# Optimization experiments

Measured on AMD Instinct MI355X. Metric: run time of the kernel, lower is better.

## Reference

```python
import jax, jax.numpy as jnp
import numpy as np

B, Q, K, D, H = 4, 2048, 2048, 512, 8
DH = D // H
MASK_VAL = -1e6


def setup_inputs() -> dict:
    key = jax.random.key(0)
    ks = jax.random.split(key, 8)
    queries = jax.random.normal(ks[0], (B, Q, D), dtype=jnp.float32)
    keys = jax.random.normal(ks[1], (B, K, D), dtype=jnp.float32)
    values = jax.random.normal(ks[2], (B, K, D), dtype=jnp.float32)
    valid_lens = jax.random.randint(ks[3], (B,), 1, K + 1, dtype=jnp.int32)
    # torch nn.Linear weights: shape [out_features, in_features], y = x @ W.T
    s = 1.0 / np.sqrt(D)
    W_q = jax.random.uniform(ks[4], (D, D), jnp.float32, -s, s)
    W_k = jax.random.uniform(ks[5], (D, D), jnp.float32, -s, s)
    W_v = jax.random.uniform(ks[6], (D, D), jnp.float32, -s, s)
    W_o = jax.random.uniform(ks[7], (D, D), jnp.float32, -s, s)
    return {"queries": queries, "keys": keys, "values": values,
            "valid_lens": valid_lens, "W_q": W_q, "W_k": W_k,
            "W_v": W_v, "W_o": W_o}


def _split_heads(x):
    # [B, S, D] -> [B, H, S, DH]
    b, s, _ = x.shape
    return x.reshape(b, s, H, DH).transpose(0, 2, 1, 3)


def reference(queries, keys, values, valid_lens, W_q, W_k, W_v, W_o):
    q = _split_heads(queries @ W_q.T)   # [B,H,Q,DH]
    k = _split_heads(keys @ W_k.T)      # [B,H,K,DH]
    v = _split_heads(values @ W_v.T)    # [B,H,K,DH]
    scores = jnp.einsum("bhqd,bhkd->bhqk", q, k) / jnp.sqrt(jnp.float32(DH))
    # padding mask: key position < valid_len[b], broadcast over heads & queries
    mask = jnp.arange(K)[None, None, None, :] < valid_lens[:, None, None, None]
    scores = jnp.where(mask, scores, MASK_VAL)
    attn = jax.nn.softmax(scores, axis=-1)  # dropout=eval/no-op
    out = jnp.einsum("bhqk,bhkd->bhqd", attn, v)
    out = out.transpose(0, 2, 1, 3).reshape(queries.shape[0], q.shape[2], D)
    return out @ W_o.T
```

## Files before the change

### kernel.cpp

```cpp
#include <hip/hip_runtime.h>
#include <cstdint>
#include <cstddef>

#define BB  4
#define QQ  2048
#define SK  2048
#define DD  512
#define HH  8
#define DHH 64

typedef __bf16 bf16;
typedef bf16  bf16x8 __attribute__((ext_vector_type(8)));
typedef bf16  bf16x4 __attribute__((ext_vector_type(4)));
typedef float f32x4  __attribute__((ext_vector_type(4)));
typedef uint32_t u32x4 __attribute__((ext_vector_type(4)));

__device__ __forceinline__ void async16(void* lds, const void* g) {
  __builtin_amdgcn_global_load_lds(
      (const __attribute__((address_space(1))) unsigned int*)g,
      (__attribute__((address_space(3))) unsigned int*)lds, 16, 0, 0);
}

__device__ __forceinline__ uint32_t pk2(float lo, float hi) {
  return __builtin_amdgcn_perm(__builtin_bit_cast(uint32_t, hi),
                               __builtin_bit_cast(uint32_t, lo), 0x07060302u);
}

__global__ __launch_bounds__(256) void cvt_w(
    const float* __restrict__ w0, const float* __restrict__ w1,
    const float* __restrict__ w2, const float* __restrict__ w3,
    bf16* __restrict__ d0, bf16* __restrict__ d1, bf16* __restrict__ d2,
    bf16* __restrict__ d3, int nw4) {
  int i = blockIdx.x * 256 + threadIdx.x;
  const float* s;
  bf16* d;
  if (i < nw4)             { s = w0; d = d0; }
  else if (i < 2 * nw4)    { s = w1; d = d1; i -= nw4; }
  else if (i < 3 * nw4)    { s = w2; d = d2; i -= 2 * nw4; }
  else if (i < 4 * nw4)    { s = w3; d = d3; i -= 3 * nw4; }
  else return;
  float4 vv = ((const float4*)s)[i];
  bf16x4 o;
  o[0] = (bf16)vv.x; o[1] = (bf16)vv.y; o[2] = (bf16)vv.z; o[3] = (bf16)vv.w;
  ((bf16x4*)d)[i] = o;
}

template <int MT, int F32S, typename EpiF>
__device__ __forceinline__ void gemm_body(
    const bf16* __restrict__ A, const bf16* __restrict__ B,
    const float* __restrict__ Af, const float* __restrict__ Bf,
    int tM, int tN, EpiF epi_fn) {
  static_assert(F32S == 0 || MT == 4, "f32 staging assumes 4 chunks/thread");
  __shared__ __align__(16) bf16 lA[MT * 32 * 64];
  __shared__ __align__(16) bf16 lB[128 * 64];
  const int tid  = threadIdx.x;
  const int l    = tid & 63;
  const int w    = tid >> 6;
  const int lrow = l & 15, lq = l >> 4;
  const int wm = (w >> 1) * (MT * 16), wn = (w & 1) * 64;

  float4 rg[8];
  auto loadreg = [&](int it) {
    const int kt = it * 64;
#pragma unroll
    for (int j = 0; j < 4; ++j) {
      int c = j * 256 + tid, row = c >> 3, gcc = (c & 7) ^ (row & 7);
      const float* s = (F32S == 1)
          ? &Af[(size_t)(tM + row) * DD + kt + gcc * 8]
          : &Bf[(size_t)(tN + row) * DD + kt + gcc * 8];
      rg[2 * j]     = *(const float4*)s;
      rg[2 * j + 1] = *(const float4*)(s + 4);
    }
  };
  auto writereg = [&]() {
#pragma unroll
    for (int j = 0; j < 4; ++j) {
      int c = j * 256 + tid;
      float4 a = rg[2 * j], b2 = rg[2 * j + 1];
      bf16x8 o;
      o[0] = (bf16)a.x;  o[1] = (bf16)a.y;  o[2] = (bf16)a.z;  o[3] = (bf16)a.w;
      o[4] = (bf16)b2.x; o[5] = (bf16)b2.y; o[6] = (bf16)b2.z; o[7] = (bf16)b2.w;
      if constexpr (F32S == 1) *(bf16x8*)&lA[c * 8] = o;
      else                     *(bf16x8*)&lB[c * 8] = o;
    }
  };

  f32x4 acc[MT][4] = {};
  if constexpr (F32S) loadreg(0);
  for (int it = 0; it < 8; ++it) {
    const int kt = it * 64;
    if (it) __syncthreads();
    if constexpr (F32S != 1) {
#pragma unroll
      for (int j = 0; j < MT; ++j) {
        int c = j * 256 + tid, row = c >> 3, gcc = (c & 7) ^ (row & 7);
        async16(&lA[c * 8], &A[(size_t)(tM + row) * DD + kt + gcc * 8]);
      }
    }
    if constexpr (F32S != 2) {
#pragma unroll
      for (int j = 0; j < 4; ++j) {
        int c = j * 256 + tid, row = c >> 3, gcc = (c & 7) ^ (row & 7);
        async16(&lB[c * 8], &B[(size_t)(tN + row) * DD + kt + gcc * 8]);
      }
    }
    if constexpr (F32S) writereg();
    __syncthreads();
    if constexpr (F32S) {
      if (it + 1 < 8) loadreg(it + 1);
    }

#pragma unroll
    for (int ks = 0; ks < 2; ++ks) {
      bf16x8 af[MT], bfr[4];
#pragma unroll
      for (int mt = 0; mt < MT; ++mt) {
        int row = wm + mt * 16 + lrow;
        int chunk = row * 8 + ((ks * 4 + lq) ^ (lrow & 7));
        af[mt] = *(const bf16x8*)&lA[chunk * 8];
      }
#pragma unroll
      for (int nt = 0; nt < 4; ++nt) {
        int row = wn + nt * 16 + lrow;
        int chunk = row * 8 + ((ks * 4 + lq) ^ (lrow & 7));
        bfr[nt] = *(const bf16x8*)&lB[chunk * 8];
      }
#pragma unroll
      for (int mt = 0; mt < MT; ++mt)
#pragma unroll
        for (int nt = 0; nt < 4; ++nt)
          acc[mt][nt] = __builtin_amdgcn_mfma_f32_16x16x32_bf16(
              af[mt], bfr[nt], acc[mt][nt], 0, 0, 0);
    }
  }

#pragma unroll
  for (int mt = 0; mt < MT; ++mt)
#pragma unroll
    for (int nt = 0; nt < 4; ++nt) {
      int row0 = tM + wm + mt * 16 + lq * 4;
      int col  = tN + wn + nt * 16 + lrow;
      epi_fn(acc[mt][nt], row0, col);
    }
}

__global__ __launch_bounds__(256, 3) void proj3(
    const float* __restrict__ xq, const bf16* __restrict__ wq, bf16* __restrict__ qh,
    const float* __restrict__ xk, const bf16* __restrict__ wk, bf16* __restrict__ kh,
    const float* __restrict__ xv, const bf16* __restrict__ wv, bf16* __restrict__ vt,
    float qscale) {
  const int z = blockIdx.y, x = blockIdx.x;
  if (z < 2) {
    const bf16*  A = z == 0 ? wq : wk;
    const float* Bf = z == 0 ? xq : xk;
    bf16* Cout     = z == 0 ? qh : kh;
    const float scale = z == 0 ? qscale : 1.0f;
    int tM = (x & 3) * 128, tN = (x >> 2) * 128;
    gemm_body<4, 2>(A, nullptr, nullptr, Bf, tM, tN,
                    [&](const f32x4& a, int row0, int col) {
      int b2 = col >> 11, s = col & 2047;
      int h2 = row0 >> 6, dh0 = row0 & 63;
      bf16x4 o;
#pragma unroll
      for (int r = 0; r < 4; ++r) o[r] = (bf16)(a[r] * scale);
      *(bf16x4*)&Cout[((size_t)(b2 * HH + h2) * QQ + s) * DHH + dh0] = o;
    });
  } else {
    int tM = (x >> 2) * 128, tN = (x & 3) * 128;
    gemm_body<4, 1>(nullptr, wv, xv, nullptr, tM, tN,
                    [&](const f32x4& a, int row0, int col) {
      int b2 = row0 >> 11, s0 = row0 & 2047;
      int h2 = col >> 6,  dh = col & 63;
      int tile = s0 >> 6, kk = s0 & 63;
      int g = kk >> 4, a2 = (kk >> 2) & 3;
      int idx0 = ((g >> 1) * 4 + a2) * 8 + (g & 1) * 4;
      bf16x4 o;
#pragma unroll
      for (int r = 0; r < 4; ++r) o[r] = (bf16)a[r];
      *(bf16x4*)&vt[((size_t)(b2 * HH + h2) * DHH + dh) * SK + tile * 64 + idx0] = o;
    });
  }
}

__global__ __launch_bounds__(256, 3) void proj_o(
    const bf16* __restrict__ wo, const bf16* __restrict__ ao,
    float* __restrict__ Cout) {
  const int x = blockIdx.x;
  int tM = (x & 7) * 64, tN = (x >> 3) * 128;
  gemm_body<2, 0>(wo, ao, nullptr, nullptr, tM, tN,
                  [&](const f32x4& a, int row0, int col) {
    *(float4*)&Cout[(size_t)col * DD + row0] = *(const float4*)&a;
  });
}

__global__ __launch_bounds__(256, 3) void attn_fused(
    const bf16* __restrict__ qh, const bf16* __restrict__ kh,
    const bf16* __restrict__ vt, const int* __restrict__ valid_lens,
    bf16* __restrict__ ao) {
  __shared__ __align__(16) bf16 lK[3][64 * 64];
  __shared__ __align__(16) bf16 lV[3][64 * 64];
  const int tid  = threadIdx.x;
  const int l    = tid & 63;
  const int w    = tid >> 6;
  const int lrow = l & 15, lq = l >> 4;
  const int rx   = lrow & 7;
  const int bh = blockIdx.x;
  const int b = bh >> 3, h = bh & 7;
  const int qt = blockIdx.y;
  const int vl  = valid_lens[b];
  const int nkt = (vl + 63) >> 6;

  const int q0 = qt * 128 + w * 32;
  const bf16* qbase = qh + (size_t)bh * QQ * DHH;
  const bf16* kbase = kh + (size_t)bh * SK * DHH;
  const bf16* vbase = vt + (size_t)bh * DHH * SK;

  auto stageKV = [&](int k0, int buf) {
#pragma unroll
    for (int j = 0; j < 2; ++j) {
      int c = j * 256 + tid, row = c >> 3, gcc = (c & 7) ^ (row & 7);
      async16(&lK[buf][c * 8], &kbase[(size_t)(k0 + row) * DHH + gcc * 8]);
    }
#pragma unroll
    for (int j = 0; j < 2; ++j) {
      int c = j * 256 + tid, row = c >> 3, gcc = (c & 7) ^ (row & 7);
      async16(&lV[buf][c * 8], &vbase[(size_t)row * SK + k0 + gcc * 8]);
    }
  };

  bf16x8 qf[2][2];
#pragma unroll
  for (int g = 0; g < 2; ++g)
#pragma unroll
    for (int ks = 0; ks < 2; ++ks)
      qf[g][ks] = *(const bf16x8*)
          &qbase[(size_t)(q0 + g * 16 + lrow) * DHH + ks * 32 + lq * 8];

  f32x4 acc[2][4] = {};
  float rs[2] = {0.f, 0.f};

  stageKV(0, 0);
  asm volatile("s_waitcnt vmcnt(0)" ::: "memory");

  for (int kt = 0; kt < nkt; ++kt) {
    const int bi = kt % 3;
    if (kt + 1 < nkt) {
      stageKV((kt + 1) * 64, (kt + 1) % 3);
      asm volatile("s_waitcnt vmcnt(4)" ::: "memory");
    } else {
      asm volatile("s_waitcnt vmcnt(0)" ::: "memory");
    }
    __builtin_amdgcn_s_barrier();
    asm volatile("" ::: "memory");
    const bf16* bufK = lK[bi];
    const bf16* bufV = lV[bi];
    const int k0 = kt * 64;

    f32x4 s[2][4] = {};
    __builtin_amdgcn_s_setprio(1);
#pragma unroll
    for (int ks = 0; ks < 2; ++ks) {
#pragma unroll
      for (int t = 0; t < 4; ++t) {
        int row = t * 16 + lrow;
        int chunkc = row * 8 + ((ks * 4 + lq) ^ rx);
        bf16x8 kf = *(const bf16x8*)&bufK[chunkc * 8];
#pragma unroll
        for (int g = 0; g < 2; ++g)
          s[g][t] = __builtin_amdgcn_mfma_f32_16x16x32_bf16(
              kf, qf[g][ks], s[g][t], 0, 0, 0);
      }
    }
    __builtin_amdgcn_s_setprio(0);

    if (vl < k0 + 64) {
#pragma unroll
      for (int t = 0; t < 4; ++t) {
        int kb = k0 + t * 16 + lq * 4;
#pragma unroll
        for (int r = 0; r < 4; ++r)
          if (kb + r >= vl) { s[0][t][r] = -1e30f; s[1][t][r] = -1e30f; }
      }
    }

#pragma unroll
    for (int g = 0; g < 2; ++g)
#pragma unroll
      for (int t = 0; t < 4; ++t)
#pragma unroll
        for (int r = 0; r < 4; ++r) {
          float p = __builtin_amdgcn_exp2f(s[g][t][r]);
          rs[g] += p;
          s[g][t][r] = p;
        }

#pragma unroll
    for (int p2 = 0; p2 < 2; ++p2) {
      u32x4 pu[2];
#pragma unroll
      for (int g = 0; g < 2; ++g) {
        pu[g][0] = pk2(s[g][2 * p2][0], s[g][2 * p2][1]);
        pu[g][1] = pk2(s[g][2 * p2][2], s[g][2 * p2][3]);
        pu[g][2] = pk2(s[g][2 * p2 + 1][0], s[g][2 * p2 + 1][1]);
        pu[g][3] = pk2(s[g][2 * p2 + 1][2], s[g][2 * p2 + 1][3]);
      }
      bf16x8 pb0 = __builtin_bit_cast(bf16x8, pu[0]);
      bf16x8 pb1 = __builtin_bit_cast(bf16x8, pu[1]);
      int cc = (p2 * 4 + lq) ^ rx;
      __builtin_amdgcn_s_setprio(1);
#pragma unroll
      for (int mt = 0; mt < 4; ++mt) {
        int row = mt * 16 + lrow;
        bf16x8 vf = *(const bf16x8*)&bufV[(row * 8 + cc) * 8];
        acc[0][mt] = __builtin_amdgcn_mfma_f32_16x16x32_bf16(
            vf, pb0, acc[0][mt], 0, 0, 0);
        acc[1][mt] = __builtin_amdgcn_mfma_f32_16x16x32_bf16(
            vf, pb1, acc[1][mt], 0, 0, 0);
      }
      __builtin_amdgcn_s_setprio(0);
    }
  }

#pragma unroll
  for (int g = 0; g < 2; ++g) {
    rs[g] += __shfl_xor(rs[g], 16);
    rs[g] += __shfl_xor(rs[g], 32);
  }

#pragma unroll
  for (int g = 0; g < 2; ++g) {
    float inv = 1.0f / rs[g];
    int q = q0 + g * 16 + lrow;
#pragma unroll
    for (int mt = 0; mt < 4; ++mt) {
      bf16x4 o;
#pragma unroll
      for (int r = 0; r < 4; ++r) o[r] = (bf16)(acc[g][mt][r] * inv);
      *(bf16x4*)&ao[((size_t)(b * QQ + q)) * DD + h * DHH + mt * 16 + lq * 4] = o;
    }
  }
}

extern "C" void kernel_launch(void* const* d_in, const int* in_sizes, int n_in,
                              void* d_out, int out_size, void* d_ws, size_t ws_size,
                              hipStream_t stream) {
  const float* queries    = (const float*)d_in[0];
  const float* keys       = (const float*)d_in[1];
  const float* values     = (const float*)d_in[2];
  const int*   valid_lens = (const int*)d_in[3];
  const float* W_q = (const float*)d_in[4];
  const float* W_k = (const float*)d_in[5];
  const float* W_v = (const float*)d_in[6];
  const float* W_o = (const float*)d_in[7];

  const size_t NX = (size_t)BB * QQ * DD;
  const size_t NW = (size_t)DD * DD;

  bf16* wq = (bf16*)d_ws;
  bf16* wk = wq + NW;
  bf16* wv = wk + NW;
  bf16* wo = wv + NW;
  bf16* qh = wo + NW;
  bf16* kh = qh + NX;
  bf16* vt = kh + NX;
  bf16* ao = vt + NX;

  dim3 blk(256);
  const int nw4 = (int)(NW / 4);
  cvt_w<<<dim3((4 * nw4 + 255) / 256), blk, 0, stream>>>(
      W_q, W_k, W_v, W_o, wq, wk, wv, wo, nw4);

  const float qscale = 0.125f * 1.44269504088896340736f;
  proj3<<<dim3(256, 3), blk, 0, stream>>>(queries, wq, qh, keys, wk, kh,
                                          values, wv, vt, qscale);

  attn_fused<<<dim3(BB * HH, QQ / 128), blk, 0, stream>>>(
      qh, kh, vt, valid_lens, ao);

  proj_o<<<dim3(512), blk, 0, stream>>>(wo, ao, (float*)d_out);
}
```

Baseline: 185.0 us.

## Load activation operand directly to registers, double-buffer weights in LDS

```diff
diff --git a/kernel.cpp b/kernel.cpp
--- a/kernel.cpp
+++ b/kernel.cpp
@@ -45,103 +45,78 @@
   ((bf16x4*)d)[i] = o;
 }
 
-template <int MT, int F32S, typename EpiF>
-__device__ __forceinline__ void gemm_body(
-    const bf16* __restrict__ A, const bf16* __restrict__ B,
-    const float* __restrict__ Af, const float* __restrict__ Bf,
-    int tM, int tN, EpiF epi_fn) {
-  static_assert(F32S == 0 || MT == 4, "f32 staging assumes 4 chunks/thread");
-  __shared__ __align__(16) bf16 lA[MT * 32 * 64];
-  __shared__ __align__(16) bf16 lB[128 * 64];
+template <int XSIDE, typename EpiF>
+__device__ __forceinline__ void gemm_dir_f32(
+    bf16* __restrict__ lW, const bf16* __restrict__ W,
+    const float* __restrict__ X, int tW, int tX, EpiF epi_fn) {
   const int tid  = threadIdx.x;
   const int l    = tid & 63;
   const int w    = tid >> 6;
-  const int lrow = l & 15, lq = l >> 4;
-  const int wm = (w >> 1) * (MT * 16), wn = (w & 1) * 64;
-
-  float4 rg[8];
-  auto loadreg = [&](int it) {
+  const int lrow = l & 15, lq = l >> 4, rx = lrow & 7;
+  const int wm = (w >> 1) * 64, wn = (w & 1) * 64;
+  const int wW = XSIDE ? wm : wn;
+  const int wX = XSIDE ? wn : wm;
+
+  auto stageW = [&](int it, bf16* dst) {
     const int kt = it * 64;
 #pragma unroll
     for (int j = 0; j < 4; ++j) {
       int c = j * 256 + tid, row = c >> 3, gcc = (c & 7) ^ (row & 7);
-      const float* s = (F32S == 1)
-          ? &Af[(size_t)(tM + row) * DD + kt + gcc * 8]
-          : &Bf[(size_t)(tN + row) * DD + kt + gcc * 8];
-      rg[2 * j]     = *(const float4*)s;
-      rg[2 * j + 1] = *(const float4*)(s + 4);
+      async16(&dst[c * 8], &W[(size_t)(tW + row) * DD + kt + gcc * 8]);
     }
   };
-  auto writereg = [&]() {
-#pragma unroll
-    for (int j = 0; j < 4; ++j) {
-      int c = j * 256 + tid;
-      float4 a = rg[2 * j], b2 = rg[2 * j + 1];
-      bf16x8 o;
-      o[0] = (bf16)a.x;  o[1] = (bf16)a.y;  o[2] = (bf16)a.z;  o[3] = (bf16)a.w;
-      o[4] = (bf16)b2.x; o[5] = (bf16)b2.y; o[6] = (bf16)b2.z; o[7] = (bf16)b2.w;
-      if constexpr (F32S == 1) *(bf16x8*)&lA[c * 8] = o;
-      else                     *(bf16x8*)&lB[c * 8] = o;
-    }
+
+  bf16x8 xf[2][4];
+  auto loadX = [&](int it) {
+    const int kt = it * 64;
+#pragma unroll
+    for (int ks = 0; ks < 2; ++ks)
+#pragma unroll
+      for (int t = 0; t < 4; ++t) {
+        const float* p =
+            &X[(size_t)(tX + wX + t * 16 + lrow) * DD + kt + ks * 32 + lq * 8];
+        float4 a = *(const float4*)p, b = *(const float4*)(p + 4);
+        bf16x8 o;
+        o[0] = (bf16)a.x; o[1] = (bf16)a.y; o[2] = (bf16)a.z; o[3] = (bf16)a.w;
+        o[4] = (bf16)b.x; o[5] = (bf16)b.y; o[6] = (bf16)b.z; o[7] = (bf16)b.w;
+        xf[ks][t] = o;
+      }
   };
 
-  f32x4 acc[MT][4] = {};
-  if constexpr (F32S) loadreg(0);
+  f32x4 acc[4][4] = {};
+  stageW(0, lW);
+  loadX(0);
+  __syncthreads();
   for (int it = 0; it < 8; ++it) {
-    const int kt = it * 64;
-    if (it) __syncthreads();
-    if constexpr (F32S != 1) {
-#pragma unroll
-      for (int j = 0; j < MT; ++j) {
-        int c = j * 256 + tid, row = c >> 3, gcc = (c & 7) ^ (row & 7);
-        async16(&lA[c * 8], &A[(size_t)(tM + row) * DD + kt + gcc * 8]);
-      }
-    }
-    if constexpr (F32S != 2) {
-#pragma unroll
-      for (int j = 0; j < 4; ++j) {
-        int c = j * 256 + tid, row = c >> 3, gcc = (c & 7) ^ (row & 7);
-        async16(&lB[c * 8], &B[(size_t)(tN + row) * DD + kt + gcc * 8]);
-      }
-    }
-    if constexpr (F32S) writereg();
-    __syncthreads();
-    if constexpr (F32S) {
-      if (it + 1 < 8) loadreg(it + 1);
-    }
-
+    bf16* cW = lW + (it & 1) * 8192;
+    if (it + 1 < 8) stageW(it + 1, lW + ((it + 1) & 1) * 8192);
 #pragma unroll
     for (int ks = 0; ks < 2; ++ks) {
-      bf16x8 af[MT], bfr[4];
-#pragma unroll
-      for (int mt = 0; mt < MT; ++mt) {
-        int row = wm + mt * 16 + lrow;
-        int chunk = row * 8 + ((ks * 4 + lq) ^ (lrow & 7));
-        af[mt] = *(const bf16x8*)&lA[chunk * 8];
-      }
-#pragma unroll
-      for (int nt = 0; nt < 4; ++nt) {
-        int row = wn + nt * 16 + lrow;
-        int chunk = row * 8 + ((ks * 4 + lq) ^ (lrow & 7));
-        bfr[nt] = *(const bf16x8*)&lB[chunk * 8];
-      }
-#pragma unroll
-      for (int mt = 0; mt < MT; ++mt)
+      bf16x8 wf[4];
+#pragma unroll
+      for (int t = 0; t < 4; ++t) {
+        int row = wW + t * 16 + lrow;
+        int chunk = row * 8 + ((ks * 4 + lq) ^ rx);
+        wf[t] = *(const bf16x8*)&cW[chunk * 8];
+      }
+#pragma unroll
+      for (int mt = 0; mt < 4; ++mt)
 #pragma unroll
         for (int nt = 0; nt < 4; ++nt)
           acc[mt][nt] = __builtin_amdgcn_mfma_f32_16x16x32_bf16(
-              af[mt], bfr[nt], acc[mt][nt], 0, 0, 0);
-    }
-  }
-
-#pragma unroll
-  for (int mt = 0; mt < MT; ++mt)
-#pragma unroll
-    for (int nt = 0; nt < 4; ++nt) {
-      int row0 = tM + wm + mt * 16 + lq * 4;
-      int col  = tN + wn + nt * 16 + lrow;
-      epi_fn(acc[mt][nt], row0, col);
-    }
+              XSIDE ? wf[mt] : xf[ks][mt], XSIDE ? xf[ks][nt] : wf[nt],
+              acc[mt][nt], 0, 0, 0);
+    }
+    if (it + 1 < 8) loadX(it + 1);
+    __syncthreads();
+  }
+
+  const int tM = XSIDE ? tW : tX, tN = XSIDE ? tX : tW;
+#pragma unroll
+  for (int mt = 0; mt < 4; ++mt)
+#pragma unroll
+    for (int nt = 0; nt < 4; ++nt)
+      epi_fn(acc[mt][nt], tM + wm + mt * 16 + lq * 4, tN + wn + nt * 16 + lrow);
 }
 
 __global__ __launch_bounds__(256, 3) void proj3(
@@ -149,15 +124,15 @@
     const float* __restrict__ xk, const bf16* __restrict__ wk, bf16* __restrict__ kh,
     const float* __restrict__ xv, const bf16* __restrict__ wv, bf16* __restrict__ vt,
     float qscale) {
+  __shared__ __align__(16) bf16 lW[2 * 128 * 64];
   const int z = blockIdx.y, x = blockIdx.x;
   if (z < 2) {
-    const bf16*  A = z == 0 ? wq : wk;
-    const float* Bf = z == 0 ? xq : xk;
+    const bf16*  W = z == 0 ? wq : wk;
+    const float* X = z == 0 ? xq : xk;
     bf16* Cout     = z == 0 ? qh : kh;
     const float scale = z == 0 ? qscale : 1.0f;
-    int tM = (x & 3) * 128, tN = (x >> 2) * 128;
-    gemm_body<4, 2>(A, nullptr, nullptr, Bf, tM, tN,
-                    [&](const f32x4& a, int row0, int col) {
+    int tW = (x >> 6) * 128, tX = (x & 63) * 128;
+    gemm_dir_f32<1>(lW, W, X, tW, tX, [&](const f32x4& a, int row0, int col) {
       int b2 = col >> 11, s = col & 2047;
       int h2 = row0 >> 6, dh0 = row0 & 63;
       bf16x4 o;
@@ -166,9 +141,8 @@
       *(bf16x4*)&Cout[((size_t)(b2 * HH + h2) * QQ + s) * DHH + dh0] = o;
     });
   } else {
-    int tM = (x >> 2) * 128, tN = (x & 3) * 128;
-    gemm_body<4, 1>(nullptr, wv, xv, nullptr, tM, tN,
-                    [&](const f32x4& a, int row0, int col) {
+    int tX = (x & 63) * 128, tW = (x >> 6) * 128;
+    gemm_dir_f32<0>(lW, wv, xv, tW, tX, [&](const f32x4& a, int row0, int col) {
       int b2 = row0 >> 11, s0 = row0 & 2047;
       int h2 = col >> 6,  dh = col & 63;
       int tile = s0 >> 6, kk = s0 & 63;
@@ -185,12 +159,69 @@
 __global__ __launch_bounds__(256, 3) void proj_o(
     const bf16* __restrict__ wo, const bf16* __restrict__ ao,
     float* __restrict__ Cout) {
+  __shared__ __align__(16) bf16 lW[2 * 64 * 64];
   const int x = blockIdx.x;
-  int tM = (x & 7) * 64, tN = (x >> 3) * 128;
-  gemm_body<2, 0>(wo, ao, nullptr, nullptr, tM, tN,
-                  [&](const f32x4& a, int row0, int col) {
-    *(float4*)&Cout[(size_t)col * DD + row0] = *(const float4*)&a;
-  });
+  const int tM = (x >> 6) * 64, tN = (x & 63) * 128;
+  const int tid  = threadIdx.x;
+  const int l    = tid & 63;
+  const int w    = tid >> 6;
+  const int lrow = l & 15, lq = l >> 4, rx = lrow & 7;
+  const int wm = (w >> 1) * 32, wn = (w & 1) * 64;
+
+  auto stageW = [&](int it, bf16* dst) {
+    const int kt = it * 64;
+#pragma unroll
+    for (int j = 0; j < 2; ++j) {
+      int c = j * 256 + tid, row = c >> 3, gcc = (c & 7) ^ (row & 7);
+      async16(&dst[c * 8], &wo[(size_t)(tM + row) * DD + kt + gcc * 8]);
+    }
+  };
+  bf16x8 xf[2][4];
+  auto loadX = [&](int it) {
+    const int kt = it * 64;
+#pragma unroll
+    for (int ks = 0; ks < 2; ++ks)
+#pragma unroll
+      for (int t = 0; t < 4; ++t)
+        xf[ks][t] = *(const bf16x8*)
+            &ao[(size_t)(tN + wn + t * 16 + lrow) * DD + kt + ks * 32 + lq * 8];
+  };
+
+  f32x4 acc[2][4] = {};
+  stageW(0, lW);
+  loadX(0);
+  __syncthreads();
+  for (int it = 0; it < 8; ++it) {
+    bf16* cW = lW + (it & 1) * 4096;
+    if (it + 1 < 8) stageW(it + 1, lW + ((it + 1) & 1) * 4096);
+#pragma unroll
+    for (int ks = 0; ks < 2; ++ks) {
+      bf16x8 wf[2];
+#pragma unroll
+      for (int t = 0; t < 2; ++t) {
+        int row = wm + t * 16 + lrow;
+        int chunk = row * 8 + ((ks * 4 + lq) ^ rx);
+        wf[t] = *(const bf16x8*)&cW[chunk * 8];
+      }
+#pragma unroll
+      for (int mt = 0; mt < 2; ++mt)
+#pragma unroll
+        for (int nt = 0; nt < 4; ++nt)
+          acc[mt][nt] = __builtin_amdgcn_mfma_f32_16x16x32_bf16(
+              wf[mt], xf[ks][nt], acc[mt][nt], 0, 0, 0);
+    }
+    if (it + 1 < 8) loadX(it + 1);
+    __syncthreads();
+  }
+
+#pragma unroll
+  for (int mt = 0; mt < 2; ++mt)
+#pragma unroll
+    for (int nt = 0; nt < 4; ++nt) {
+      int row0 = tM + wm + mt * 16 + lq * 4;
+      int col  = tN + wn + nt * 16 + lrow;
+      *(float4*)&Cout[(size_t)col * DD + row0] = *(const float4*)&acc[mt][nt];
+    }
 }
 
 __global__ __launch_bounds__(256, 3) void attn_fused(
```

New measurement: 202.0 us. +9.2%, slower.
